# Kernel tuning notes

Hardware: AMD Instinct MI355X
Metric: run time of the kernel (lower is better)

## Reference

```python
import jax, jax.numpy as jnp
import numpy as np

B, C_IN, C_OUT, N, T = 32, 64, 64, 1024, 16


def setup_inputs() -> dict:
    key = jax.random.key(0)
    k1, k2, k3, k4, k5 = jax.random.split(key, 5)
    x = jax.random.normal(k1, (B, C_IN, N, T), dtype=jnp.float32)
    adj = jax.random.uniform(k2, (N, N), dtype=jnp.float32)
    alpha = jax.random.normal(k3, (C_IN,), dtype=jnp.float32) * 0.1
    W_att = jax.random.normal(k4, (T, T), dtype=jnp.float32) * 0.1
    W_out = jax.random.normal(k5, (C_OUT, C_IN), dtype=jnp.float32) * 0.1
    return {"x": x, "adj": adj, "alpha": alpha, "W_att": W_att, "W_out": W_out}


def reference(x, adj, alpha, W_att, W_out):
    # x: [B, C_in, N, T]; adj: [N, N]
    # k = q = einsum('bint,i->bnt', x, alpha)
    k = jnp.einsum('bint,i->bnt', x, alpha)              # [B, N, T]
    # scores = k @ W @ q^T over timestep dim -> [B, N, N]
    scores = jnp.einsum('bnt,ts,bms->bnm', k, W_att, k)
    att = jax.nn.softmax(scores, axis=-1) * adj          # [B, N, N]
    # out = (att @ x.permute(3,0,2,1)) @ W_out.T, then permute back
    agg = jnp.einsum('bnm,bcmt->bcnt', att, x)           # [B, C_in, N, T]
    out = jnp.einsum('bcnt,oc->bont', agg, W_out)        # [B, C_out, N, T]
    return out
```

## Files before the change

kernel.cpp:

```cpp
#include <hip/hip_runtime.h>
#include <hip/hip_bf16.h>


typedef float  f32x4 __attribute__((ext_vector_type(4)));
typedef short  s16x8 __attribute__((ext_vector_type(8)));
typedef unsigned short u16x8 __attribute__((ext_vector_type(8)));

#define GLOAD_LDS16(g, l) __builtin_amdgcn_global_load_lds(                    \
    (const __attribute__((address_space(1))) void*)(g),                        \
    (__attribute__((address_space(3))) void*)(l), 16, 0, 0)

static __device__ __forceinline__ unsigned short f2bf(float f) {
    __hip_bfloat16 h = __float2bfloat16(f);
    return *reinterpret_cast<unsigned short*>(&h);
}

__global__ __launch_bounds__(256) void kCF(const float* __restrict__ x,
                                           const float* __restrict__ Wout,
                                           const float* __restrict__ alpha,
                                           const float* __restrict__ Watt,
                                           unsigned short* __restrict__ ybf,
                                           float* __restrict__ kk_,
                                           float* __restrict__ kq_) {
    __shared__ __align__(16) float Xt[64][68];
    __shared__ __align__(16) float WT[64][68];
    __shared__ float al[64];
    __shared__ float wl[16][17];
    __shared__ float kl[64];
    int tid = threadIdx.x;
    int b = blockIdx.x >> 8;
    int j0 = (blockIdx.x & 255) * 64;
    if (tid < 64) al[tid] = alpha[tid];
    wl[tid >> 4][tid & 15] = Watt[tid];
    #pragma unroll
    for (int it = 0; it < 16; ++it) {
        int idx = it * 256 + tid;
        int o = idx >> 6, c = idx & 63;
        WT[c][o] = Wout[idx];
        int c2 = it * 4 + (tid >> 6), j = tid & 63;
        Xt[c2][j] = x[(size_t)(b * 64 + c2) * 16384 + j0 + j];
    }
    __syncthreads();
    int oy = tid >> 4, jx = tid & 15;
    float acc[4][4] = {};
    #pragma unroll
    for (int c = 0; c < 64; ++c) {
        float4 w4 = *(const float4*)&WT[c][oy * 4];
        float4 x4 = *(const float4*)&Xt[c][jx * 4];
        float wv[4] = {w4.x, w4.y, w4.z, w4.w};
        float xv[4] = {x4.x, x4.y, x4.z, x4.w};
        #pragma unroll
        for (int u = 0; u < 4; ++u)
            #pragma unroll
            for (int v = 0; v < 4; ++v)
                acc[u][v] = fmaf(wv[u], xv[v], acc[u][v]);
    }
    #pragma unroll
    for (int u = 0; u < 4; ++u) {
        int o = oy * 4 + u;
        ushort4 w4 = make_ushort4(f2bf(acc[u][0]), f2bf(acc[u][1]),
                                  f2bf(acc[u][2]), f2bf(acc[u][3]));
        *(ushort4*)&ybf[(size_t)(b * 64 + o) * 16384 + j0 + jx * 4] = w4;
    }
    if (tid < 64) {
        float kv = 0.f;
        #pragma unroll
        for (int c = 0; c < 64; ++c) kv = fmaf(al[c], Xt[c][tid], kv);
        kl[tid] = kv;
    }
    __syncthreads();
    if (tid < 64) {
        int mq = tid >> 4, tq = tid & 15;
        float q = 0.f;
        #pragma unroll
        for (int s = 0; s < 16; ++s) q = fmaf(kl[mq * 16 + s], wl[s][tq], q);
        size_t gj = (size_t)b * 16384 + j0 + tid;
        kk_[gj] = kl[tid];
        kq_[gj] = q;
    }
}

__global__ __launch_bounds__(256) void kBP(const float* __restrict__ kk_,
                                           const float* __restrict__ kq_,
                                           const float* __restrict__ adj,
                                           unsigned short* __restrict__ Pbf) {
    int tid = threadIdx.x;
    int b  = blockIdx.x >> 8;
    int n0 = (blockIdx.x & 255) * 4;
    __shared__ float kql[4][16];
    __shared__ float redm[4][4], reds[4][4];
    if (tid < 64)
        kql[tid >> 4][tid & 15] =
            kq_[((size_t)b * 1024 + n0 + (tid >> 4)) * 16 + (tid & 15)];
    __syncthreads();
    const float* kb = kk_ + (size_t)b * 16384;
    float kf[4][16];
    #pragma unroll
    for (int u = 0; u < 4; ++u) {
        const float* p = &kb[(size_t)(u * 256 + tid) * 16];
        #pragma unroll
        for (int s = 0; s < 16; ++s) kf[u][s] = p[s];
    }
    float sc[4][4];
    #pragma unroll
    for (int r = 0; r < 4; ++r)
        #pragma unroll
        for (int u = 0; u < 4; ++u) {
            float a = 0.f;
            #pragma unroll
            for (int s = 0; s < 16; ++s) a = fmaf(kql[r][s], kf[u][s], a);
            sc[r][u] = a;
        }
    float mx[4];
    #pragma unroll
    for (int r = 0; r < 4; ++r)
        mx[r] = fmaxf(fmaxf(sc[r][0], sc[r][1]), fmaxf(sc[r][2], sc[r][3]));
    #pragma unroll
    for (int off = 32; off; off >>= 1)
        #pragma unroll
        for (int r = 0; r < 4; ++r) mx[r] = fmaxf(mx[r], __shfl_xor(mx[r], off));
    int w = tid >> 6;
    if ((tid & 63) == 0)
        #pragma unroll
        for (int r = 0; r < 4; ++r) redm[w][r] = mx[r];
    __syncthreads();
    #pragma unroll
    for (int r = 0; r < 4; ++r)
        mx[r] = fmaxf(fmaxf(redm[0][r], redm[1][r]), fmaxf(redm[2][r], redm[3][r]));
    float e[4][4], se[4];
    #pragma unroll
    for (int r = 0; r < 4; ++r) {
        float s = 0.f;
        #pragma unroll
        for (int u = 0; u < 4; ++u) { e[r][u] = __expf(sc[r][u] - mx[r]); s += e[r][u]; }
        se[r] = s;
    }
    #pragma unroll
    for (int off = 32; off; off >>= 1)
        #pragma unroll
        for (int r = 0; r < 4; ++r) se[r] += __shfl_xor(se[r], off);
    if ((tid & 63) == 0)
        #pragma unroll
        for (int r = 0; r < 4; ++r) reds[w][r] = se[r];
    __syncthreads();
    float rrs[4];
    #pragma unroll
    for (int r = 0; r < 4; ++r)
        rrs[r] = 1.f / (reds[0][r] + reds[1][r] + reds[2][r] + reds[3][r]);
    #pragma unroll
    for (int r = 0; r < 4; ++r)
        #pragma unroll
        for (int u = 0; u < 4; ++u) {
            size_t m = (size_t)u * 256 + tid;
            float av = adj[(size_t)(n0 + r) * 1024 + m];
            Pbf[((size_t)b * 1024 + n0 + r) * 1024 + m] = f2bf(e[r][u] * rrs[r] * av);
        }
}

__global__ __launch_bounds__(256) void kT(const unsigned short* __restrict__ ybf,
                                          unsigned short* __restrict__ Yt) {
    __shared__ unsigned short Tl[64][72];
    int tid = threadIdx.x;
    int mc = blockIdx.x, oc = blockIdx.y, b = blockIdx.z;
    int oo = tid >> 6, mm = tid & 63;
    const unsigned short* src =
        ybf + ((size_t)(b * 64 + oc * 4 + oo) * 1024 + mc * 64 + mm) * 16;
    u16x8 v0 = *(const u16x8*)src;
    u16x8 v1 = *(const u16x8*)(src + 8);
    #pragma unroll
    for (int t = 0; t < 8; ++t) Tl[oo * 16 + t][mm] = v0[t];
    #pragma unroll
    for (int t = 0; t < 8; ++t) Tl[oo * 16 + 8 + t][mm] = v1[t];
    __syncthreads();
    int j = tid >> 2, ms = (tid & 3) * 16;
    u16x8 o0, o1;
    #pragma unroll
    for (int q = 0; q < 8; ++q) { o0[q] = Tl[j][ms + q]; o1[q] = Tl[j][ms + 8 + q]; }
    unsigned short* dst = Yt + (((size_t)b * 1024 + oc * 64 + j) << 10) + mc * 64 + ms;
    *(u16x8*)dst = o0;
    *(u16x8*)(dst + 8) = o1;
}

static __device__ __forceinline__ void stage_tile(const unsigned short* Pb,
                                                  const unsigned short* Yb,
                                                  unsigned short* lds, int buf,
                                                  int kt, int ww, int l) {
    int r8  = (l >> 3) & 7;
    int glc = ((l & 7) ^ r8) << 3;
    int k0  = kt << 6;
    unsigned short* base = lds + buf * 32768;
    #pragma unroll
    for (int s = 0; s < 4; ++s) {
        int row  = s * 64 + ww * 8;
        size_t g = ((size_t)(row + r8) << 10) + k0 + glc;
        GLOAD_LDS16(Pb + g, base + row * 64);
        GLOAD_LDS16(Yb + g, base + 16384 + row * 64);
    }
}

static __device__ __forceinline__ s16x8 frag_ld(const unsigned short* base,
                                                int R, int kc, int l7) {
    return *(const s16x8*)(base + R * 64 + ((kc ^ l7) << 3));
}

__global__ __launch_bounds__(512, 2) void kD(const unsigned short* __restrict__ P,
                                             const unsigned short* __restrict__ Yt,
                                             float* __restrict__ out) {
    extern __shared__ unsigned short lds[];
    int bid = blockIdx.x;
    int wg  = (bid & 7) * 64 + (bid >> 3);
    int b   = wg >> 4;
    int rem = wg & 15;
    int n0  = (rem & 3) << 8;
    int j0  = (rem >> 2) << 8;
    int tid = threadIdx.x;
    int l = tid & 63, ww = tid >> 6;
    int wr = ww >> 2, wc = ww & 3;
    int l15 = l & 15, lhi = l >> 4, l7 = l & 7;
    const unsigned short* Pb = P  + ((size_t)b << 20) + ((size_t)n0 << 10);
    const unsigned short* Yb = Yt + ((size_t)b << 20) + ((size_t)j0 << 10);

    f32x4 acc[8][4] = {};
    stage_tile(Pb, Yb, lds, 0, 0, ww, l);
    __syncthreads();

    for (int kt = 0; kt < 16; ++kt) {
        int cur = kt & 1;
        const unsigned short* Ab = lds + cur * 32768;
        const unsigned short* Bb = Ab + 16384;
        s16x8 bf[4][2];
        #pragma unroll
        for (int q = 0; q < 4; ++q) {
            if (q == 0) {
                int ktn = kt < 15 ? kt + 1 : 15;
                stage_tile(Pb, Yb, lds, cur ^ 1, ktn, ww, l);
                #pragma unroll
                for (int nj = 0; nj < 4; ++nj)
                    #pragma unroll
                    for (int ks = 0; ks < 2; ++ks)
                        bf[nj][ks] = frag_ld(Bb, wc * 64 + nj * 16 + l15,
                                             ks * 4 + lhi, l7);
            }
            s16x8 af[2][2];
            #pragma unroll
            for (int mi = 0; mi < 2; ++mi)
                #pragma unroll
                for (int ks = 0; ks < 2; ++ks)
                    af[mi][ks] = frag_ld(Ab, wr * 128 + (q * 2 + mi) * 16 + l15,
                                         ks * 4 + lhi, l7);
            __builtin_amdgcn_s_barrier();
            asm volatile("s_waitcnt lgkmcnt(0)" ::: "memory");
            __builtin_amdgcn_sched_barrier(0);
            __builtin_amdgcn_s_setprio(1);
            #pragma unroll
            for (int mi = 0; mi < 2; ++mi)
                #pragma unroll
                for (int nj = 0; nj < 4; ++nj)
                    #pragma unroll
                    for (int ks = 0; ks < 2; ++ks)
                        acc[q * 2 + mi][nj] = __builtin_amdgcn_mfma_f32_16x16x32_bf16(
                            af[mi][ks], bf[nj][ks], acc[q * 2 + mi][nj], 0, 0, 0);
            __builtin_amdgcn_s_setprio(0);
            if (q < 3) __builtin_amdgcn_s_barrier();
        }
        __syncthreads();
    }

    #pragma unroll
    for (int mi = 0; mi < 8; ++mi)
        #pragma unroll
        for (int nj = 0; nj < 4; ++nj) {
            int o  = (j0 >> 4) + wc * 4 + nj;
            int nb = n0 + wr * 128 + mi * 16 + lhi * 4;
            float* op = out + ((size_t)(b * 64 + o) << 14) + (size_t)nb * 16 + l15;
            #pragma unroll
            for (int q = 0; q < 4; ++q) op[q * 16] = acc[mi][nj][q];
        }
}

extern "C" void kernel_launch(void* const* d_in, const int* in_sizes, int n_in,
                              void* d_out, int out_size, void* d_ws, size_t ws_size,
                              hipStream_t stream) {
    const float* x     = (const float*)d_in[0];
    const float* adj   = (const float*)d_in[1];
    const float* alpha = (const float*)d_in[2];
    const float* Watt  = (const float*)d_in[3];
    const float* Wout  = (const float*)d_in[4];
    float* out = (float*)d_out;

    char* ws = (char*)d_ws;
    float* k  = (float*)ws;
    float* kq = (float*)(ws + 2097152);
    unsigned short* r1 = (unsigned short*)(ws + 4194304);
    unsigned short* r2 = (unsigned short*)(ws + 4194304 + 67108864);

    kCF<<<8192, 256, 0, stream>>>(x, Wout, alpha, Watt, r1, k, kq);
    kT <<<dim3(16, 16, 32), 256, 0, stream>>>(r1, r2);
    kBP<<<8192, 256, 0, stream>>>(k, kq, adj, r1);
    kD <<<512, 512, 131072, stream>>>(r1, r2, out);
}
```

Baseline: 234.0 us.

## Fuse channel-mix with transpose via MFMA and triple-buffer the main GEMM

```diff
diff --git a/kernel.cpp b/kernel.cpp
--- a/kernel.cpp
+++ b/kernel.cpp
@@ -15,68 +15,106 @@
     return *reinterpret_cast<unsigned short*>(&h);
 }
 
-__global__ __launch_bounds__(256) void kCF(const float* __restrict__ x,
+__global__ __launch_bounds__(256) void kCM(const float* __restrict__ x,
                                            const float* __restrict__ Wout,
                                            const float* __restrict__ alpha,
                                            const float* __restrict__ Watt,
-                                           unsigned short* __restrict__ ybf,
+                                           unsigned short* __restrict__ Yt,
                                            float* __restrict__ kk_,
                                            float* __restrict__ kq_) {
-    __shared__ __align__(16) float Xt[64][68];
-    __shared__ __align__(16) float WT[64][68];
-    __shared__ float al[64];
-    __shared__ float wl[16][17];
-    __shared__ float kl[64];
+    extern __shared__ char sm[];
+    float* xt = (float*)sm;
+    unsigned short* Ys = (unsigned short*)sm;
+    unsigned short* Wb = (unsigned short*)(sm + 66560);
+    float* al = (float*)(sm + 75776);
+    float* wl = (float*)(sm + 76032);
+    float* kl = (float*)(sm + 77120);
     int tid = threadIdx.x;
-    int b = blockIdx.x >> 8;
-    int j0 = (blockIdx.x & 255) * 64;
+    int b  = blockIdx.x >> 6;
+    int mc = blockIdx.x & 63;
+    int j0 = mc << 8;
+    int m0 = mc << 4;
     if (tid < 64) al[tid] = alpha[tid];
-    wl[tid >> 4][tid & 15] = Watt[tid];
+    wl[(tid >> 4) * 17 + (tid & 15)] = Watt[tid];
     #pragma unroll
     for (int it = 0; it < 16; ++it) {
         int idx = it * 256 + tid;
-        int o = idx >> 6, c = idx & 63;
-        WT[c][o] = Wout[idx];
-        int c2 = it * 4 + (tid >> 6), j = tid & 63;
-        Xt[c2][j] = x[(size_t)(b * 64 + c2) * 16384 + j0 + j];
-    }
-    __syncthreads();
-    int oy = tid >> 4, jx = tid & 15;
-    float acc[4][4] = {};
-    #pragma unroll
-    for (int c = 0; c < 64; ++c) {
-        float4 w4 = *(const float4*)&WT[c][oy * 4];
-        float4 x4 = *(const float4*)&Xt[c][jx * 4];
-        float wv[4] = {w4.x, w4.y, w4.z, w4.w};
-        float xv[4] = {x4.x, x4.y, x4.z, x4.w};
-        #pragma unroll
-        for (int u = 0; u < 4; ++u)
-            #pragma unroll
-            for (int v = 0; v < 4; ++v)
-                acc[u][v] = fmaf(wv[u], xv[v], acc[u][v]);
-    }
-    #pragma unroll
-    for (int u = 0; u < 4; ++u) {
-        int o = oy * 4 + u;
-        ushort4 w4 = make_ushort4(f2bf(acc[u][0]), f2bf(acc[u][1]),
-                                  f2bf(acc[u][2]), f2bf(acc[u][3]));
-        *(ushort4*)&ybf[(size_t)(b * 64 + o) * 16384 + j0 + jx * 4] = w4;
-    }
-    if (tid < 64) {
+        Wb[(idx >> 6) * 72 + (idx & 63)] = f2bf(Wout[idx]);
+    }
+    const float* xb = x + (size_t)b * (64 * 16384) + j0;
+    #pragma unroll
+    for (int it = 0; it < 16; ++it) {
+        int idx = it * 256 + tid;
+        int c = idx >> 6, j4 = (idx & 63) << 2;
+        float4 v = *(const float4*)(xb + (size_t)c * 16384 + j4);
+        *(float4*)&xt[c * 260 + j4] = v;
+    }
+    __syncthreads();
+    int w = tid >> 6, l = tid & 63;
+    int l15 = l & 15, lhi = l >> 4;
+    int jw = w << 6;
+    f32x4 acc[4][4] = {};
+    s16x8 af[4][2];
+    #pragma unroll
+    for (int fro = 0; fro < 4; ++fro)
+        #pragma unroll
+        for (int ks = 0; ks < 2; ++ks)
+            af[fro][ks] = *(const s16x8*)&Wb[(fro * 16 + l15) * 72 + ks * 32 + lhi * 8];
+    #pragma unroll
+    for (int fc = 0; fc < 4; ++fc) {
+        #pragma unroll
+        for (int ks = 0; ks < 2; ++ks) {
+            int jcol = jw + fc * 16 + l15;
+            int cb = ks * 32 + lhi * 8;
+            s16x8 bf;
+            #pragma unroll
+            for (int e = 0; e < 8; ++e)
+                bf[e] = (short)f2bf(xt[(cb + e) * 260 + jcol]);
+            #pragma unroll
+            for (int fro = 0; fro < 4; ++fro)
+                acc[fro][fc] = __builtin_amdgcn_mfma_f32_16x16x32_bf16(
+                    af[fro][ks], bf, acc[fro][fc], 0, 0, 0);
+        }
+    }
+    {
         float kv = 0.f;
         #pragma unroll
-        for (int c = 0; c < 64; ++c) kv = fmaf(al[c], Xt[c][tid], kv);
+        for (int c = 0; c < 64; ++c) kv = fmaf(al[c], xt[c * 260 + tid], kv);
         kl[tid] = kv;
-    }
-    __syncthreads();
-    if (tid < 64) {
-        int mq = tid >> 4, tq = tid & 15;
+        kk_[(size_t)b * 16384 + j0 + tid] = kv;
+    }
+    __syncthreads();
+    {
+        int ml = tid >> 4, tq = tid & 15;
         float q = 0.f;
         #pragma unroll
-        for (int s = 0; s < 16; ++s) q = fmaf(kl[mq * 16 + s], wl[s][tq], q);
-        size_t gj = (size_t)b * 16384 + j0 + tid;
-        kk_[gj] = kl[tid];
-        kq_[gj] = q;
+        for (int s = 0; s < 16; ++s) q = fmaf(kl[ml * 16 + s], wl[s * 17 + tq], q);
+        kq_[(size_t)b * 16384 + j0 + tid] = q;
+    }
+    #pragma unroll
+    for (int fro = 0; fro < 4; ++fro)
+        #pragma unroll
+        for (int fc = 0; fc < 4; ++fc) {
+            int jl = jw + fc * 16 + l15;
+            int o0 = fro * 16 + lhi * 4;
+            ushort4 pk = make_ushort4(f2bf(acc[fro][fc][0]), f2bf(acc[fro][fc][1]),
+                                      f2bf(acc[fro][fc][2]), f2bf(acc[fro][fc][3]));
+            *(ushort4*)&Ys[jl * 72 + o0] = pk;
+        }
+    __syncthreads();
+    #pragma unroll
+    for (int it = 0; it < 4; ++it) {
+        int r = it * 256 + tid;
+        int o = r >> 4, t = r & 15;
+        u16x8 v0, v1;
+        #pragma unroll
+        for (int q = 0; q < 8; ++q) {
+            v0[q] = Ys[(q * 16 + t) * 72 + o];
+            v1[q] = Ys[((q + 8) * 16 + t) * 72 + o];
+        }
+        unsigned short* dst = Yt + (((size_t)b << 10) + r) * 1024 + m0;
+        *(u16x8*)dst = v0;
+        *(u16x8*)(dst + 8) = v1;
     }
 }
 
@@ -157,50 +195,28 @@
         }
 }
 
-__global__ __launch_bounds__(256) void kT(const unsigned short* __restrict__ ybf,
-                                          unsigned short* __restrict__ Yt) {
-    __shared__ unsigned short Tl[64][72];
-    int tid = threadIdx.x;
-    int mc = blockIdx.x, oc = blockIdx.y, b = blockIdx.z;
-    int oo = tid >> 6, mm = tid & 63;
-    const unsigned short* src =
-        ybf + ((size_t)(b * 64 + oc * 4 + oo) * 1024 + mc * 64 + mm) * 16;
-    u16x8 v0 = *(const u16x8*)src;
-    u16x8 v1 = *(const u16x8*)(src + 8);
-    #pragma unroll
-    for (int t = 0; t < 8; ++t) Tl[oo * 16 + t][mm] = v0[t];
-    #pragma unroll
-    for (int t = 0; t < 8; ++t) Tl[oo * 16 + 8 + t][mm] = v1[t];
-    __syncthreads();
-    int j = tid >> 2, ms = (tid & 3) * 16;
-    u16x8 o0, o1;
-    #pragma unroll
-    for (int q = 0; q < 8; ++q) { o0[q] = Tl[j][ms + q]; o1[q] = Tl[j][ms + 8 + q]; }
-    unsigned short* dst = Yt + (((size_t)b * 1024 + oc * 64 + j) << 10) + mc * 64 + ms;
-    *(u16x8*)dst = o0;
-    *(u16x8*)(dst + 8) = o1;
-}
-
-static __device__ __forceinline__ void stage_tile(const unsigned short* Pb,
-                                                  const unsigned short* Yb,
-                                                  unsigned short* lds, int buf,
-                                                  int kt, int ww, int l) {
-    int r8  = (l >> 3) & 7;
-    int glc = ((l & 7) ^ r8) << 3;
-    int k0  = kt << 6;
-    unsigned short* base = lds + buf * 32768;
-    #pragma unroll
-    for (int s = 0; s < 4; ++s) {
-        int row  = s * 64 + ww * 8;
-        size_t g = ((size_t)(row + r8) << 10) + k0 + glc;
-        GLOAD_LDS16(Pb + g, base + row * 64);
-        GLOAD_LDS16(Yb + g, base + 16384 + row * 64);
-    }
-}
-
-static __device__ __forceinline__ s16x8 frag_ld(const unsigned short* base,
-                                                int R, int kc, int l7) {
-    return *(const s16x8*)(base + R * 64 + ((kc ^ l7) << 3));
+static __device__ __forceinline__ void stage32(const unsigned short* Pb,
+                                               const unsigned short* Yb,
+                                               unsigned short* lds, int buf,
+                                               int kt, int ww, int l) {
+    int S  = ((l >> 2) ^ (l >> 4)) & 3;
+    int cs = (((l & 3) ^ S)) << 3;
+    int k0 = kt << 5;
+    unsigned short* base = lds + buf * 16384;
+    #pragma unroll
+    for (int s = 0; s < 2; ++s) {
+        int rbase = s * 128 + ww * 16;
+        size_t g = ((size_t)(rbase + (l >> 2)) << 10) + k0 + cs;
+        GLOAD_LDS16(Pb + g, base + rbase * 32);
+        GLOAD_LDS16(Yb + g, base + 8192 + rbase * 32);
+    }
+}
+
+static __device__ __forceinline__ s16x8 frag32(const unsigned short* base,
+                                               int row, int l) {
+    int S = (row ^ (row >> 2)) & 3;
+    int g = (l >> 4) & 3;
+    return *(const s16x8*)(base + row * 32 + ((g ^ S) << 3));
 }
 
 __global__ __launch_bounds__(512, 2) void kD(const unsigned short* __restrict__ P,
@@ -216,54 +232,55 @@
     int tid = threadIdx.x;
     int l = tid & 63, ww = tid >> 6;
     int wr = ww >> 2, wc = ww & 3;
-    int l15 = l & 15, lhi = l >> 4, l7 = l & 7;
+    int l15 = l & 15, lhi = l >> 4;
     const unsigned short* Pb = P  + ((size_t)b << 20) + ((size_t)n0 << 10);
     const unsigned short* Yb = Yt + ((size_t)b << 20) + ((size_t)j0 << 10);
 
     f32x4 acc[8][4] = {};
-    stage_tile(Pb, Yb, lds, 0, 0, ww, l);
-    __syncthreads();
-
-    for (int kt = 0; kt < 16; ++kt) {
-        int cur = kt & 1;
-        const unsigned short* Ab = lds + cur * 32768;
-        const unsigned short* Bb = Ab + 16384;
-        s16x8 bf[4][2];
-        #pragma unroll
-        for (int q = 0; q < 4; ++q) {
-            if (q == 0) {
-                int ktn = kt < 15 ? kt + 1 : 15;
-                stage_tile(Pb, Yb, lds, cur ^ 1, ktn, ww, l);
-                #pragma unroll
-                for (int nj = 0; nj < 4; ++nj)
-                    #pragma unroll
-                    for (int ks = 0; ks < 2; ++ks)
-                        bf[nj][ks] = frag_ld(Bb, wc * 64 + nj * 16 + l15,
-                                             ks * 4 + lhi, l7);
-            }
-            s16x8 af[2][2];
-            #pragma unroll
-            for (int mi = 0; mi < 2; ++mi)
-                #pragma unroll
-                for (int ks = 0; ks < 2; ++ks)
-                    af[mi][ks] = frag_ld(Ab, wr * 128 + (q * 2 + mi) * 16 + l15,
-                                         ks * 4 + lhi, l7);
-            __builtin_amdgcn_s_barrier();
-            asm volatile("s_waitcnt lgkmcnt(0)" ::: "memory");
-            __builtin_amdgcn_sched_barrier(0);
-            __builtin_amdgcn_s_setprio(1);
-            #pragma unroll
-            for (int mi = 0; mi < 2; ++mi)
-                #pragma unroll
-                for (int nj = 0; nj < 4; ++nj)
-                    #pragma unroll
-                    for (int ks = 0; ks < 2; ++ks)
-                        acc[q * 2 + mi][nj] = __builtin_amdgcn_mfma_f32_16x16x32_bf16(
-                            af[mi][ks], bf[nj][ks], acc[q * 2 + mi][nj], 0, 0, 0);
-            __builtin_amdgcn_s_setprio(0);
-            if (q < 3) __builtin_amdgcn_s_barrier();
-        }
-        __syncthreads();
+    stage32(Pb, Yb, lds, 0, 0, ww, l);
+    stage32(Pb, Yb, lds, 1, 1, ww, l);
+
+    for (int kt = 0; kt < 32; ++kt) {
+        int cur = kt % 3;
+        const unsigned short* Ab = lds + cur * 16384;
+        const unsigned short* Bb = Ab + 8192;
+        if (kt < 31) asm volatile("s_waitcnt vmcnt(4)" ::: "memory");
+        else         asm volatile("s_waitcnt vmcnt(0)" ::: "memory");
+        __builtin_amdgcn_s_barrier();
+        s16x8 bf[4], af0[4];
+        #pragma unroll
+        for (int nj = 0; nj < 4; ++nj)
+            bf[nj] = frag32(Bb, wc * 64 + nj * 16 + l15, l);
+        #pragma unroll
+        for (int mi = 0; mi < 4; ++mi)
+            af0[mi] = frag32(Ab, wr * 128 + mi * 16 + l15, l);
+        if (kt < 30) stage32(Pb, Yb, lds, (kt + 2) % 3, kt + 2, ww, l);
+        __builtin_amdgcn_s_barrier();
+        asm volatile("s_waitcnt lgkmcnt(0)" ::: "memory");
+        __builtin_amdgcn_sched_barrier(0);
+        __builtin_amdgcn_s_setprio(1);
+        #pragma unroll
+        for (int mi = 0; mi < 4; ++mi)
+            #pragma unroll
+            for (int nj = 0; nj < 4; ++nj)
+                acc[mi][nj] = __builtin_amdgcn_mfma_f32_16x16x32_bf16(
+                    af0[mi], bf[nj], acc[mi][nj], 0, 0, 0);
+        __builtin_amdgcn_s_setprio(0);
+        __builtin_amdgcn_s_barrier();
+        s16x8 af1[4];
+        #pragma unroll
+        for (int mi = 0; mi < 4; ++mi)
+            af1[mi] = frag32(Ab, wr * 128 + (4 + mi) * 16 + l15, l);
+        asm volatile("s_waitcnt lgkmcnt(0)" ::: "memory");
+        __builtin_amdgcn_sched_barrier(0);
+        __builtin_amdgcn_s_setprio(1);
+        #pragma unroll
+        for (int mi = 0; mi < 4; ++mi)
+            #pragma unroll
+            for (int nj = 0; nj < 4; ++nj)
+                acc[4 + mi][nj] = __builtin_amdgcn_mfma_f32_16x16x32_bf16(
+                    af1[mi], bf[nj], acc[4 + mi][nj], 0, 0, 0);
+        __builtin_amdgcn_s_setprio(0);
     }
 
     #pragma unroll
@@ -291,11 +308,10 @@
     char* ws = (char*)d_ws;
     float* k  = (float*)ws;
     float* kq = (float*)(ws + 2097152);
-    unsigned short* r1 = (unsigned short*)(ws + 4194304);
-    unsigned short* r2 = (unsigned short*)(ws + 4194304 + 67108864);
-
-    kCF<<<8192, 256, 0, stream>>>(x, Wout, alpha, Watt, r1, k, kq);
-    kT <<<dim3(16, 16, 32), 256, 0, stream>>>(r1, r2);
-    kBP<<<8192, 256, 0, stream>>>(k, kq, adj, r1);
-    kD <<<512, 512, 131072, stream>>>(r1, r2, out);
-}
+    unsigned short* Pbf = (unsigned short*)(ws + 4194304);
+    unsigned short* Yt  = (unsigned short*)(ws + 4194304 + 67108864);
+
+    kCM<<<2048, 256, 78144, stream>>>(x, Wout, alpha, Watt, Yt, k, kq);
+    kBP<<<8192, 256, 0, stream>>>(k, kq, adj, Pbf);
+    kD <<<512, 512, 98304, stream>>>(Pbf, Yt, out);
+}
```

Result: faster. 202.0 us (-13.7%).
